# Optimization experiments

Measured on AMD Instinct MI355X. Metric: run time of the kernel, lower is better.

Reference implementation:

```python
import jax, jax.numpy as jnp
import numpy as np

B = 256        # graphs
NODES = 116    # nodes per view per graph
FEAT = 115     # node feature dim
LENN = 6670    # edges per view per graph (116*115/2)
SEG2 = 13456   # raw edges per graph in input (2*LENN + 116 discarded)
HID = 128      # hidden_channels
HC = 512       # hc


def setup_inputs() -> dict:
    key = jax.random.key(0)
    ks = jax.random.split(key, 12)
    x = jax.random.normal(ks[0], (B * 2 * NODES, FEAT), jnp.float32)
    # per-graph edge layout: [6670 FC edges | 6670 SC edges | 116 dummy]
    off = (2 * NODES) * jnp.arange(B, dtype=jnp.int32)  # [B]
    fc = jax.random.randint(ks[1], (2, B, LENN), 0, NODES, dtype=jnp.int32) + off[None, :, None]
    sc = jax.random.randint(ks[2], (2, B, LENN), 0, NODES, dtype=jnp.int32) + off[None, :, None] + NODES
    dummy = jnp.zeros((2, B, SEG2 - 2 * LENN), jnp.int32) + off[None, :, None]
    edge_index = jnp.concatenate([fc, sc, dummy], axis=2).reshape(2, B * SEG2)
    edge_weight = jax.random.uniform(ks[3], (B * SEG2,), jnp.float32)
    batch = jnp.repeat(jnp.arange(B, dtype=jnp.int32), 2 * NODES)
    s = 1.0 / np.sqrt(FEAT)
    W1 = jax.random.uniform(ks[4], (FEAT, HID), jnp.float32, -s, s)
    b1 = jnp.zeros((HID,), jnp.float32)
    W2 = jax.random.uniform(ks[5], (FEAT, HID), jnp.float32, -s, s)
    b2 = jnp.zeros((HID,), jnp.float32)
    s6 = 1.0 / np.sqrt(2 * NODES)
    W6 = jax.random.uniform(ks[6], (2 * NODES, HC), jnp.float32, -s6, s6)
    b6 = jax.random.uniform(ks[7], (HC,), jnp.float32, -s6, s6)
    s7 = 1.0 / np.sqrt(HC)
    W7 = jax.random.uniform(ks[8], (HC, 1), jnp.float32, -s7, s7)
    b7 = jax.random.uniform(ks[9], (1,), jnp.float32, -s7, s7)
    return dict(x=x, edge_index=edge_index, edge_weight=edge_weight, batch=batch,
                W1=W1, b1=b1, W2=W2, b2=b2, W6=W6, b6=b6, W7=W7, b7=b7)


def _gcn_conv(x, ei, ew, W, b, num_nodes):
    """PyG GCNConv: D^-1/2 (A+I) D^-1/2 X W + b (self-loop weight 1)."""
    h = x @ W                                   # [N, HID]
    src, dst = ei[0], ei[1]
    deg = jax.ops.segment_sum(ew, dst, num_segments=num_nodes) + 1.0  # +1 self-loop
    dinv = jax.lax.rsqrt(deg)                   # [N]
    norm = dinv[src] * ew * dinv[dst]           # [E]
    out = jax.ops.segment_sum(h[src] * norm[:, None], dst, num_segments=num_nodes)
    out = out + (dinv * dinv)[:, None] * h      # self-loop message
    return out + b


def reference(x, edge_index, edge_weight, batch, W1, b1, W2, b2, W6, b6, W7, b7):
    gidx = jnp.arange(B, dtype=edge_index.dtype)
    ei = edge_index.reshape(2, B, SEG2)
    ew = edge_weight.reshape(B, SEG2)
    # de-offset per-graph edges into per-view node index spaces (116 nodes/graph)
    ei_fc = (ei[:, :, :LENN] - NODES * gidx[None, :, None]).reshape(2, B * LENN)
    ei_sc = (ei[:, :, LENN:2 * LENN] - NODES * (gidx + 1)[None, :, None]).reshape(2, B * LENN)
    ew_fc = ew[:, :LENN].reshape(-1)
    ew_sc = ew[:, LENN:2 * LENN].reshape(-1)
    xr = x.reshape(B, 2 * NODES, FEAT)
    node_fc = xr[:, :NODES].reshape(B * NODES, FEAT)
    node_sc = xr[:, NODES:].reshape(B * NODES, FEAT)
    N = B * NODES
    x1 = _gcn_conv(node_fc, ei_fc, ew_fc, W1, b1, N).max(axis=1)  # [B*116]
    x2 = _gcn_conv(node_sc, ei_sc, ew_sc, W2, b2, N).max(axis=1)  # [B*116]
    feat = jnp.stack([x1, x2], axis=1).reshape(B, 2 * NODES)      # flatten()
    # dropout p=0.5 is identity in eval mode
    h = jax.nn.relu(feat @ W6 + b6)
    return h @ W7 + b7  # [B, 1]
```

## Files before the change

### kernel.cpp

```cpp
#include <hip/hip_runtime.h>


#define NB 256
#define NODES 116
#define FEAT 115
#define LENN 6670
#define SEG2 13456
#define HID 128
#define HC 512
#define AF_STR 117

typedef float f32x4 __attribute__((ext_vector_type(4)));
typedef short short8 __attribute__((ext_vector_type(8)));
typedef __bf16 bf16x8 __attribute__((ext_vector_type(8)));

#define MFMA16(a, b, c) __builtin_amdgcn_mfma_f32_16x16x32_bf16( \
    __builtin_bit_cast(bf16x8, (a)), __builtin_bit_cast(bf16x8, (b)), (c), 0, 0, 0)

#define OFF_ALO 32768
#define OFF_BHI 65536
#define OFF_BLO 98304
#define OFF_PMAX 131072
#define OFF_DINV 133120
#define LDS_BYTES 133632

__device__ __forceinline__ unsigned f2bf(float f) {
  unsigned u = __builtin_bit_cast(unsigned, f);
  return (u + 0x7FFFu + ((u >> 16) & 1u)) >> 16;
}
__device__ __forceinline__ float bf2f(unsigned h) {
  return __builtin_bit_cast(float, h << 16);
}
__device__ __forceinline__ void cvt2(float v0, float v1, unsigned& hi, unsigned& lo) {
  unsigned h0 = f2bf(v0), h1 = f2bf(v1);
  hi = h0 | (h1 << 16);
  lo = f2bf(v0 - bf2f(h0)) | (f2bf(v1 - bf2f(h1)) << 16);
}
__device__ __forceinline__ int kperm(int k) {
  return (k & ~31) | (k & 3) | (((k >> 2) & 3) << 3) | (((k >> 4) & 1) << 2);
}
__device__ __forceinline__ int swzb(int row, int kbyte) {
  return row * 256 + (kbyte ^ ((row & 7) << 4));
}
__device__ __forceinline__ f32x4 splat4(float f) {
  f32x4 r = {f, f, f, f};
  return r;
}

__global__ __launch_bounds__(1024, 1) void k_fused(
    const float* __restrict__ x, const int* __restrict__ ei,
    const float* __restrict__ ew,
    const float* __restrict__ W1, const float* __restrict__ b1,
    const float* __restrict__ W2, const float* __restrict__ b2,
    float* __restrict__ featws)
{
  __shared__ __align__(16) char sm[LDS_BYTES];
  float* Afp   = (float*)(sm + OFF_BHI);
  float* dinv  = (float*)(sm + OFF_DINV);
  float* pmaxp = (float*)(sm + OFF_PMAX);
  const int bid = blockIdx.x;
  const int g = bid >> 1, v = bid & 1;
  const int tid = threadIdx.x;

  {
    f32x4 z = splat4(0.f);
    f32x4* p = (f32x4*)(sm + OFF_BHI);
    for (int i = tid; i < 3393; i += 1024) p[i] = z;
  }
  __syncthreads();

  const int eoff = g * SEG2 + v * LENN;
  const int nbase = g * 232 + v * 116;

  {
    const int* __restrict__ srcp = ei + eoff;
    const int* __restrict__ dstp = ei + (size_t)NB * SEG2 + eoff;
    const float* __restrict__ wp = ew + eoff;
    for (int q = tid; q < (LENN / 2); q += 1024) {
      int2 s2 = ((const int2*)srcp)[q];
      int2 d2 = ((const int2*)dstp)[q];
      float2 w2 = ((const float2*)wp)[q];
      atomicAdd(&Afp[(d2.x - nbase) * AF_STR + (s2.x - nbase)], w2.x);
      atomicAdd(&Afp[(d2.y - nbase) * AF_STR + (s2.y - nbase)], w2.y);
    }
  }
  __syncthreads();

  if (tid < 4 * NODES) {
    const int r = tid >> 2, q = tid & 3;
    const float* row = Afp + r * AF_STR + q * 29;
    float s = 0.f;
#pragma unroll
    for (int j = 0; j < 29; ++j) s += row[j];
    s += __shfl_xor(s, 1, 64);
    s += __shfl_xor(s, 2, 64);
    if (q == 0) dinv[r] = rsqrtf(s + 1.0f);
  }
  __syncthreads();

  for (int p = tid; p < NODES * 64; p += 1024) {
    const int row = p >> 6;
    const int c0 = (p & 63) << 1, c1 = c0 + 1;
    const float dr = dinv[row];
    float t0 = 0.f, t1 = 0.f;
    if (c0 < NODES) {
      t0 = Afp[row * AF_STR + c0] * (dr * dinv[c0]);
      if (c0 == row) t0 += dr * dr;
    }
    if (c1 < NODES) {
      t1 = Afp[row * AF_STR + c1] * (dr * dinv[c1]);
      if (c1 == row) t1 += dr * dr;
    }
    unsigned hi, lo;
    cvt2(t0, t1, hi, lo);
    const int byte = swzb(row, kperm(c0) << 1);
    *(unsigned*)(sm + byte) = hi;
    *(unsigned*)(sm + OFF_ALO + byte) = lo;
  }
  __syncthreads();

  {
    const float* __restrict__ xg = x + (size_t)nbase * FEAT;
#pragma unroll
    for (int i = 0; i < 8; ++i) {
      int unit = tid + (i << 10);
      int sp = unit >> 7, c = unit & 127;
      int s0 = sp << 1, s1 = s0 + 1;
      float x0 = (c < FEAT && s0 < NODES) ? xg[s0 * FEAT + c] : 0.f;
      float x1 = (c < FEAT && s1 < NODES) ? xg[s1 * FEAT + c] : 0.f;
      unsigned hi, lo;
      cvt2(x0, x1, hi, lo);
      int byte = swzb(c, kperm(s0) << 1);
      *(unsigned*)(sm + OFF_BHI + byte) = hi;
      *(unsigned*)(sm + OFF_BLO + byte) = lo;
    }
  }
  __syncthreads();

  const int lane = tid & 63, w = tid >> 6;
  const int mg = w >> 2, ng = w & 3;
  const int rA0 = (mg << 5) + (lane & 15), rA1 = rA0 + 16;
  const int rB0 = (ng << 5) + (lane & 15), rB1 = rB0 + 16;
  const int kb = (lane >> 4) << 4;

  f32x4 acc00 = splat4(0.f), acc01 = splat4(0.f);
  f32x4 acc10 = splat4(0.f), acc11 = splat4(0.f);

#pragma unroll
  for (int kc = 0; kc < 4; ++kc) {
    const int ko = (kc << 6) + kb;
    short8 a0h = *(const short8*)(sm + swzb(rA0, ko));
    short8 a0l = *(const short8*)(sm + OFF_ALO + swzb(rA0, ko));
    short8 a1h = *(const short8*)(sm + swzb(rA1, ko));
    short8 a1l = *(const short8*)(sm + OFF_ALO + swzb(rA1, ko));
    short8 b0h = *(const short8*)(sm + OFF_BHI + swzb(rB0, ko));
    short8 b0l = *(const short8*)(sm + OFF_BLO + swzb(rB0, ko));
    short8 b1h = *(const short8*)(sm + OFF_BHI + swzb(rB1, ko));
    short8 b1l = *(const short8*)(sm + OFF_BLO + swzb(rB1, ko));
    acc00 = MFMA16(a0h, b0h, acc00); acc00 = MFMA16(a0l, b0h, acc00); acc00 = MFMA16(a0h, b0l, acc00);
    acc01 = MFMA16(a0h, b1h, acc01); acc01 = MFMA16(a0l, b1h, acc01); acc01 = MFMA16(a0h, b1l, acc01);
    acc10 = MFMA16(a1h, b0h, acc10); acc10 = MFMA16(a1l, b0h, acc10); acc10 = MFMA16(a1h, b0l, acc10);
    acc11 = MFMA16(a1h, b1h, acc11); acc11 = MFMA16(a1l, b1h, acc11); acc11 = MFMA16(a1h, b1l, acc11);
  }
  __syncthreads();

  {
#pragma unroll
    for (int mt = 0; mt < 2; ++mt)
#pragma unroll
      for (int nt = 0; nt < 2; ++nt)
#pragma unroll
        for (int r2 = 0; r2 < 4; ++r2) {
          f32x4 a = (mt == 0) ? (nt == 0 ? acc00 : acc01)
                              : (nt == 0 ? acc10 : acc11);
          float f = a[r2];
          int row = (mg << 5) + (mt << 4) + ((lane >> 4) << 2) + r2;
          int col = (ng << 5) + (nt << 4) + (lane & 15);
          unsigned hi = f2bf(f);
          unsigned lo = f2bf(f - bf2f(hi));
          int byte = swzb(row, kperm(col) << 1);
          *(unsigned short*)(sm + byte) = (unsigned short)hi;
          *(unsigned short*)(sm + OFF_ALO + byte) = (unsigned short)lo;
        }
    const float* __restrict__ Wv = v ? W2 : W1;
#pragma unroll
    for (int i = 0; i < 8; ++i) {
      int unit = tid + (i << 10);
      int kp = unit >> 7, c = unit & 127;
      int k0 = kp << 1, k1 = k0 + 1;
      float w0 = (k0 < FEAT) ? Wv[(size_t)k0 * HID + c] : 0.f;
      float w1 = (k1 < FEAT) ? Wv[(size_t)k1 * HID + c] : 0.f;
      unsigned hi, lo;
      cvt2(w0, w1, hi, lo);
      int byte = swzb(c, kperm(k0) << 1);
      *(unsigned*)(sm + OFF_BHI + byte) = hi;
      *(unsigned*)(sm + OFF_BLO + byte) = lo;
    }
  }
  __syncthreads();

  {
    const float* __restrict__ bv = v ? b2 : b1;
    float bb0 = bv[(ng << 5) + (lane & 15)];
    float bb1 = bv[(ng << 5) + 16 + (lane & 15)];
    acc00 = splat4(bb0); acc01 = splat4(bb1);
    acc10 = splat4(bb0); acc11 = splat4(bb1);
  }
#pragma unroll
  for (int kc = 0; kc < 4; ++kc) {
    const int ko = (kc << 6) + kb;
    short8 a0h = *(const short8*)(sm + swzb(rA0, ko));
    short8 a0l = *(const short8*)(sm + OFF_ALO + swzb(rA0, ko));
    short8 a1h = *(const short8*)(sm + swzb(rA1, ko));
    short8 a1l = *(const short8*)(sm + OFF_ALO + swzb(rA1, ko));
    short8 b0h = *(const short8*)(sm + OFF_BHI + swzb(rB0, ko));
    short8 b0l = *(const short8*)(sm + OFF_BLO + swzb(rB0, ko));
    short8 b1h = *(const short8*)(sm + OFF_BHI + swzb(rB1, ko));
    short8 b1l = *(const short8*)(sm + OFF_BLO + swzb(rB1, ko));
    acc00 = MFMA16(a0h, b0h, acc00); acc00 = MFMA16(a0l, b0h, acc00); acc00 = MFMA16(a0h, b0l, acc00);
    acc01 = MFMA16(a0h, b1h, acc01); acc01 = MFMA16(a0l, b1h, acc01); acc01 = MFMA16(a0h, b1l, acc01);
    acc10 = MFMA16(a1h, b0h, acc10); acc10 = MFMA16(a1l, b0h, acc10); acc10 = MFMA16(a1h, b0l, acc10);
    acc11 = MFMA16(a1h, b1h, acc11); acc11 = MFMA16(a1l, b1h, acc11); acc11 = MFMA16(a1h, b1l, acc11);
  }

#pragma unroll
  for (int mt = 0; mt < 2; ++mt)
#pragma unroll
    for (int r2 = 0; r2 < 4; ++r2) {
      f32x4 aN0 = (mt == 0) ? acc00 : acc10;
      f32x4 aN1 = (mt == 0) ? acc01 : acc11;
      float m = fmaxf(aN0[r2], aN1[r2]);
      m = fmaxf(m, __shfl_xor(m, 1, 64));
      m = fmaxf(m, __shfl_xor(m, 2, 64));
      m = fmaxf(m, __shfl_xor(m, 4, 64));
      m = fmaxf(m, __shfl_xor(m, 8, 64));
      if ((lane & 15) == 0) {
        int row = (mg << 5) + (mt << 4) + ((lane >> 4) << 2) + r2;
        pmaxp[(ng << 7) + row] = m;
      }
    }
  __syncthreads();
  if (tid < NODES) {
    float m = fmaxf(fmaxf(pmaxp[tid], pmaxp[128 + tid]),
                    fmaxf(pmaxp[256 + tid], pmaxp[384 + tid]));
    featws[g * 232 + 2 * tid + v] = m;
  }
}

__global__ __launch_bounds__(1024) void k_mlp(
    const float* __restrict__ featws, const float* __restrict__ W6,
    const float* __restrict__ b6, const float* __restrict__ W7,
    const float* __restrict__ b7, float* __restrict__ out)
{
  __shared__ float sf[232];
  __shared__ float ph[512];
  __shared__ float red[8];
  const int g = blockIdx.x, tid = threadIdx.x;
  if (tid < 232) sf[tid] = featws[g * 232 + tid];
  __syncthreads();

  const int col = tid & 511, half = tid >> 9;
  const float* __restrict__ w6p = W6 + (size_t)(half * 116) * HC + col;
  const float* __restrict__ sfh = sf + half * 116;
  float p = 0.f;
#pragma unroll 4
  for (int k = 0; k < 116; ++k)
    p = fmaf(sfh[k], w6p[(size_t)k * HC], p);
  if (half) ph[col] = p;
  __syncthreads();

  if (!half) {
    float a = b6[col] + p + ph[col];
    a = fmaxf(a, 0.f) * W7[col];
#pragma unroll
    for (int off = 32; off >= 1; off >>= 1) a += __shfl_xor(a, off, 64);
    if ((tid & 63) == 0) red[tid >> 6] = a;
  }
  __syncthreads();
  if (tid == 0) {
    float t = b7[0];
#pragma unroll
    for (int i = 0; i < 8; ++i) t += red[i];
    out[g] = t;
  }
}

extern "C" void kernel_launch(void* const* d_in, const int* in_sizes, int n_in,
                              void* d_out, int out_size, void* d_ws, size_t ws_size,
                              hipStream_t stream)
{
  const float* x  = (const float*)d_in[0];
  const int*   ei = (const int*)d_in[1];
  const float* ew = (const float*)d_in[2];
  const float* W1 = (const float*)d_in[4];
  const float* b1 = (const float*)d_in[5];
  const float* W2 = (const float*)d_in[6];
  const float* b2 = (const float*)d_in[7];
  const float* W6 = (const float*)d_in[8];
  const float* b6 = (const float*)d_in[9];
  const float* W7 = (const float*)d_in[10];
  const float* b7 = (const float*)d_in[11];

  float* featws = (float*)d_ws;
  float* out    = (float*)d_out;

  hipLaunchKernelGGL(k_fused, dim3(2 * NB), dim3(1024), 0, stream,
                     x, ei, ew, W1, b1, W2, b2, featws);
  hipLaunchKernelGGL(k_mlp,   dim3(NB),     dim3(1024), 0, stream,
                     featws, W6, b6, W7, b7, out);
}
```

Baseline: 171.5 us.

## Prefetch X and W into registers early and widen bf16 split stores to 8 bytes

The X tile is now loaded from global into registers before the A-normalisation pass, and the weights are loaded before the first MFMA loop, so their latency overlaps with LDS work and compute. Conversion now handles 4 consecutive k values per thread and writes 8-byte uint2 stores using a new kb64 permutation. Manual round-to-nearest-even bit math is replaced by the hardware __bf16 cast. This costs about 32 extra live registers per thread at 1024 threads per block, which may cause spills.

```diff
diff --git a/kernel.cpp b/kernel.cpp
--- a/kernel.cpp
+++ b/kernel.cpp
@@ -24,20 +24,29 @@
 #define OFF_DINV 133120
 #define LDS_BYTES 133632
 
-__device__ __forceinline__ unsigned f2bf(float f) {
-  unsigned u = __builtin_bit_cast(unsigned, f);
-  return (u + 0x7FFFu + ((u >> 16) & 1u)) >> 16;
-}
-__device__ __forceinline__ float bf2f(unsigned h) {
-  return __builtin_bit_cast(float, h << 16);
-}
-__device__ __forceinline__ void cvt2(float v0, float v1, unsigned& hi, unsigned& lo) {
-  unsigned h0 = f2bf(v0), h1 = f2bf(v1);
-  hi = h0 | (h1 << 16);
-  lo = f2bf(v0 - bf2f(h0)) | (f2bf(v1 - bf2f(h1)) << 16);
+__device__ __forceinline__ unsigned short f2bf_s(float f) {
+  return __builtin_bit_cast(unsigned short, (__bf16)f);
+}
+__device__ __forceinline__ float bf2f_s(unsigned short h) {
+  return __builtin_bit_cast(float, (unsigned)h << 16);
+}
+__device__ __forceinline__ void cvt4(const float* v, uint2& hi, uint2& lo) {
+  unsigned short h[4], l[4];
+#pragma unroll
+  for (int j = 0; j < 4; ++j) {
+    h[j] = f2bf_s(v[j]);
+    l[j] = f2bf_s(v[j] - bf2f_s(h[j]));
+  }
+  hi.x = (unsigned)h[0] | ((unsigned)h[1] << 16);
+  hi.y = (unsigned)h[2] | ((unsigned)h[3] << 16);
+  lo.x = (unsigned)l[0] | ((unsigned)l[1] << 16);
+  lo.y = (unsigned)l[2] | ((unsigned)l[3] << 16);
 }
 __device__ __forceinline__ int kperm(int k) {
   return (k & ~31) | (k & 3) | (((k >> 2) & 3) << 3) | (((k >> 4) & 1) << 2);
+}
+__device__ __forceinline__ int kb64(int t) {
+  return ((t & 3) << 4) | (((t >> 2) & 1) << 3) | ((t >> 3) << 6);
 }
 __device__ __forceinline__ int swzb(int row, int kbyte) {
   return row * 256 + (kbyte ^ ((row & 7) << 4));
@@ -98,42 +107,53 @@
   }
   __syncthreads();
 
-  for (int p = tid; p < NODES * 64; p += 1024) {
-    const int row = p >> 6;
-    const int c0 = (p & 63) << 1, c1 = c0 + 1;
-    const float dr = dinv[row];
-    float t0 = 0.f, t1 = 0.f;
-    if (c0 < NODES) {
-      t0 = Afp[row * AF_STR + c0] * (dr * dinv[c0]);
-      if (c0 == row) t0 += dr * dr;
-    }
-    if (c1 < NODES) {
-      t1 = Afp[row * AF_STR + c1] * (dr * dinv[c1]);
-      if (c1 == row) t1 += dr * dr;
-    }
-    unsigned hi, lo;
-    cvt2(t0, t1, hi, lo);
-    const int byte = swzb(row, kperm(c0) << 1);
-    *(unsigned*)(sm + byte) = hi;
-    *(unsigned*)(sm + OFF_ALO + byte) = lo;
-  }
-  __syncthreads();
-
+  float xr[4][4];
   {
     const float* __restrict__ xg = x + (size_t)nbase * FEAT;
 #pragma unroll
-    for (int i = 0; i < 8; ++i) {
-      int unit = tid + (i << 10);
-      int sp = unit >> 7, c = unit & 127;
-      int s0 = sp << 1, s1 = s0 + 1;
-      float x0 = (c < FEAT && s0 < NODES) ? xg[s0 * FEAT + c] : 0.f;
-      float x1 = (c < FEAT && s1 < NODES) ? xg[s1 * FEAT + c] : 0.f;
-      unsigned hi, lo;
-      cvt2(x0, x1, hi, lo);
-      int byte = swzb(c, kperm(s0) << 1);
-      *(unsigned*)(sm + OFF_BHI + byte) = hi;
-      *(unsigned*)(sm + OFF_BLO + byte) = lo;
-    }
+    for (int i = 0; i < 4; ++i) {
+      int u = tid + (i << 10);
+      int t = u >> 7, c = u & 127;
+#pragma unroll
+      for (int j = 0; j < 4; ++j) {
+        int s = 4 * t + j;
+        xr[i][j] = (c < FEAT && s < NODES) ? xg[s * FEAT + c] : 0.f;
+      }
+    }
+  }
+
+  for (int p = tid; p < NODES * 32; p += 1024) {
+    const int row = p >> 5;
+    const int t = p & 31;
+    const int c = t << 2;
+    float tv[4] = {0.f, 0.f, 0.f, 0.f};
+    if (t < 29) {
+      const float dr = dinv[row];
+#pragma unroll
+      for (int j = 0; j < 4; ++j) {
+        const int cc = c + j;
+        float q = Afp[row * AF_STR + cc] * (dr * dinv[cc]);
+        if (cc == row) q += dr * dr;
+        tv[j] = q;
+      }
+    }
+    uint2 hi, lo;
+    cvt4(tv, hi, lo);
+    const int byte = swzb(row, kb64(t));
+    *(uint2*)(sm + byte) = hi;
+    *(uint2*)(sm + OFF_ALO + byte) = lo;
+  }
+  __syncthreads();
+
+#pragma unroll
+  for (int i = 0; i < 4; ++i) {
+    int u = tid + (i << 10);
+    int t = u >> 7, c = u & 127;
+    uint2 hi, lo;
+    cvt4(xr[i], hi, lo);
+    int byte = swzb(c, kb64(t));
+    *(uint2*)(sm + OFF_BHI + byte) = hi;
+    *(uint2*)(sm + OFF_BLO + byte) = lo;
   }
   __syncthreads();
 
@@ -142,6 +162,21 @@
   const int rA0 = (mg << 5) + (lane & 15), rA1 = rA0 + 16;
   const int rB0 = (ng << 5) + (lane & 15), rB1 = rB0 + 16;
   const int kb = (lane >> 4) << 4;
+
+  float wr[4][4];
+  {
+    const float* __restrict__ Wv = v ? W2 : W1;
+#pragma unroll
+    for (int i = 0; i < 4; ++i) {
+      int u = tid + (i << 10);
+      int t = u >> 7, c = u & 127;
+#pragma unroll
+      for (int j = 0; j < 4; ++j) {
+        int k = 4 * t + j;
+        wr[i][j] = (k < FEAT) ? Wv[(size_t)k * HID + c] : 0.f;
+      }
+    }
+  }
 
   f32x4 acc00 = splat4(0.f), acc01 = splat4(0.f);
   f32x4 acc10 = splat4(0.f), acc11 = splat4(0.f);
@@ -176,25 +211,21 @@
           float f = a[r2];
           int row = (mg << 5) + (mt << 4) + ((lane >> 4) << 2) + r2;
           int col = (ng << 5) + (nt << 4) + (lane & 15);
-          unsigned hi = f2bf(f);
-          unsigned lo = f2bf(f - bf2f(hi));
+          unsigned short hi = f2bf_s(f);
+          unsigned short lo = f2bf_s(f - bf2f_s(hi));
           int byte = swzb(row, kperm(col) << 1);
-          *(unsigned short*)(sm + byte) = (unsigned short)hi;
-          *(unsigned short*)(sm + OFF_ALO + byte) = (unsigned short)lo;
+          *(unsigned short*)(sm + byte) = hi;
+          *(unsigned short*)(sm + OFF_ALO + byte) = lo;
         }
-    const float* __restrict__ Wv = v ? W2 : W1;
-#pragma unroll
-    for (int i = 0; i < 8; ++i) {
-      int unit = tid + (i << 10);
-      int kp = unit >> 7, c = unit & 127;
-      int k0 = kp << 1, k1 = k0 + 1;
-      float w0 = (k0 < FEAT) ? Wv[(size_t)k0 * HID + c] : 0.f;
-      float w1 = (k1 < FEAT) ? Wv[(size_t)k1 * HID + c] : 0.f;
-      unsigned hi, lo;
-      cvt2(w0, w1, hi, lo);
-      int byte = swzb(c, kperm(k0) << 1);
-      *(unsigned*)(sm + OFF_BHI + byte) = hi;
-      *(unsigned*)(sm + OFF_BLO + byte) = lo;
+#pragma unroll
+    for (int i = 0; i < 4; ++i) {
+      int u = tid + (i << 10);
+      int t = u >> 7, c = u & 127;
+      uint2 hi, lo;
+      cvt4(wr[i], hi, lo);
+      int byte = swzb(c, kb64(t));
+      *(uint2*)(sm + OFF_BHI + byte) = hi;
+      *(uint2*)(sm + OFF_BLO + byte) = lo;
     }
   }
   __syncthreads();
```

Result: faster. 157.6 us (-8.1%).
